# Performance work log

Measured on AMD Instinct MI355X. Metric: run time of the kernel, lower is better.

The kernel has to match this reference:

```python
import jax, jax.numpy as jnp
import numpy as np

EMBED_DIM = 1024
N_HEADS = 16
D_HEAD = EMBED_DIM // N_HEADS


def setup_inputs() -> dict:
    key = jax.random.key(0)
    kx, kq, kk, kv = jax.random.split(key, 4)
    x = jax.random.normal(kx, (2, 2048, EMBED_DIM), dtype=jnp.float32)
    Wq = jax.random.normal(kq, (EMBED_DIM, EMBED_DIM), dtype=jnp.float32) * 0.02
    Wk = jax.random.normal(kk, (EMBED_DIM, EMBED_DIM), dtype=jnp.float32) * 0.02
    Wv = jax.random.normal(kv, (EMBED_DIM, EMBED_DIM), dtype=jnp.float32) * 0.02
    return {"x": x, "Wq": Wq, "Wk": Wk, "Wv": Wv}


def reference(x, Wq, Wk, Wv):
    B, N, D = x.shape
    H, Dh = N_HEADS, D_HEAD
    # Fused QKV projections, then split heads: [B, N, D] -> [B, H, N, Dh]
    q = (x @ Wq).reshape(B, N, H, Dh).transpose(0, 2, 1, 3)
    k = (x @ Wk).reshape(B, N, H, Dh).transpose(0, 2, 1, 3)
    v = (x @ Wv).reshape(B, N, H, Dh).transpose(0, 2, 1, 3)
    scale = 1.0 / jnp.sqrt(jnp.asarray(Dh, dtype=x.dtype))
    scores = jnp.einsum("bhqd,bhkd->bhqk", q, k) * scale  # [B, H, N, N]
    attn = jax.nn.softmax(scores, axis=-1)
    out = jnp.einsum("bhqk,bhkd->bhqd", attn, v)  # [B, H, N, Dh]
    return out.transpose(0, 2, 1, 3).reshape(B, N, D)
```

## Files before the change

kernel.cpp:

```cpp
#include <hip/hip_runtime.h>
#include <cstdint>

typedef __bf16 bf16;
typedef __bf16 bf16x8 __attribute__((ext_vector_type(8)));
typedef float floatx4 __attribute__((ext_vector_type(4)));

typedef const __attribute__((address_space(1))) void* as1_cvptr;
typedef __attribute__((address_space(3))) void* as3_vptr;

__device__ __forceinline__ void gl_lds16(const void* g, void* l) {
  __builtin_amdgcn_global_load_lds((as1_cvptr)(uintptr_t)g,
                                   (as3_vptr)(uint32_t)(uintptr_t)l, 16, 0, 0);
}

#define EMBED 1024
#define SEQ 2048
#define NH 16
#define DH 64

__global__ __launch_bounds__(256) void convert_x(const float* __restrict__ x,
                                                 bf16* __restrict__ xb) {
  int i = (blockIdx.x * 256 + threadIdx.x) * 8;
  floatx4 a = *(const floatx4*)(x + i);
  floatx4 b = *(const floatx4*)(x + i + 4);
  bf16x8 o;
#pragma unroll
  for (int j = 0; j < 4; ++j) { o[j] = (bf16)a[j]; o[4 + j] = (bf16)b[j]; }
  *(bf16x8*)(xb + i) = o;
}

__global__ __launch_bounds__(256) void transpose3(
    const float* __restrict__ Wq, const float* __restrict__ Wk,
    const float* __restrict__ Wv, bf16* __restrict__ Wqt,
    bf16* __restrict__ Wkt, bf16* __restrict__ Wvt) {
  __shared__ __align__(16) bf16 tile[64][72];
  const float* W;
  bf16* Wt;
  if (blockIdx.z == 0) { W = Wq; Wt = Wqt; }
  else if (blockIdx.z == 1) { W = Wk; Wt = Wkt; }
  else { W = Wv; Wt = Wvt; }
  int t = threadIdx.x;
  int k0 = blockIdx.y * 64, n0 = blockIdx.x * 64;
  int r = t >> 3, c = (t & 7) * 8;
#pragma unroll
  for (int half = 0; half < 2; ++half) {
    const float* src = &W[(size_t)(k0 + r + half * 32) * EMBED + n0 + c];
    floatx4 f0 = *(const floatx4*)src;
    floatx4 f1 = *(const floatx4*)(src + 4);
    bf16x8 o;
#pragma unroll
    for (int j = 0; j < 4; ++j) { o[j] = (bf16)f0[j]; o[4 + j] = (bf16)f1[j]; }
    *(bf16x8*)&tile[r + half * 32][c] = o;
  }
  __syncthreads();
#pragma unroll
  for (int p = 0; p < 2; ++p) {
    int nn = (t >> 3) + p * 32, kk = (t & 7) * 8;
    bf16x8 v;
#pragma unroll
    for (int i = 0; i < 8; ++i) v[i] = tile[kk + i][nn];
    *(bf16x8*)&Wt[(size_t)(n0 + nn) * EMBED + k0 + kk] = v;
  }
}

__global__ __launch_bounds__(256) void qkv3(
    const bf16* __restrict__ Xb, const bf16* __restrict__ Wqt,
    const bf16* __restrict__ Wkt, const bf16* __restrict__ Wvt,
    bf16* __restrict__ qo, bf16* __restrict__ ko, bf16* __restrict__ vto) {
  __shared__ __align__(16) bf16 As[128 * 32];
  __shared__ __align__(16) bf16 Bs[128 * 32];

  int gid = blockIdx.x;
  int z = gid % 3;
  int rem = gid / 3;
  int bxx = rem & 7, byy = rem >> 3;

  const bf16* Wt = (z == 0) ? Wqt : (z == 1) ? Wkt : Wvt;
  bf16* out = (z == 0) ? qo : (z == 1) ? ko : vto;
  int m0 = (z == 2 ? bxx : byy) * 128;
  int n0 = (z == 2 ? byy : bxx) * 128;
  const bf16* Asrc = (z == 2) ? Wt : Xb;
  const bf16* Bsrc = (z == 2) ? Xb : Wt;

  int t = threadIdx.x;
  int w = t >> 6, lane = t & 63, ln = lane & 15, quad = lane >> 4;
  int wm = (w >> 1) * 64, wn = (w & 1) * 64;

  floatx4 acc[4][4];
#pragma unroll
  for (int i = 0; i < 4; ++i)
#pragma unroll
    for (int j = 0; j < 4; ++j) acc[i][j] = floatx4{0.f, 0.f, 0.f, 0.f};

  int sr = t >> 2, sc = (t & 3) * 8;
  const bf16* ag = Asrc + (size_t)(m0 + sr) * EMBED + sc;
  const bf16* bg = Bsrc + (size_t)(n0 + sr) * EMBED + sc;
  bf16* al = As + sr * 32 + sc;
  bf16* bl = Bs + sr * 32 + sc;

  for (int k0 = 0; k0 < EMBED; k0 += 32) {
    __syncthreads();
    gl_lds16(ag + k0, al);
    gl_lds16(ag + k0 + (size_t)64 * EMBED, al + 64 * 32);
    gl_lds16(bg + k0, bl);
    gl_lds16(bg + k0 + (size_t)64 * EMBED, bl + 64 * 32);
    __syncthreads();

    bf16x8 afr[4], bfr[4];
#pragma unroll
    for (int i = 0; i < 4; ++i)
      afr[i] = *(const bf16x8*)&As[(wm + i * 16 + ln) * 32 + quad * 8];
#pragma unroll
    for (int j = 0; j < 4; ++j)
      bfr[j] = *(const bf16x8*)&Bs[(wn + j * 16 + ln) * 32 + quad * 8];
#pragma unroll
    for (int i = 0; i < 4; ++i)
#pragma unroll
      for (int j = 0; j < 4; ++j)
        acc[i][j] =
            __builtin_amdgcn_mfma_f32_16x16x32_bf16(afr[i], bfr[j], acc[i][j], 0, 0, 0);
  }

#pragma unroll
  for (int i = 0; i < 4; ++i) {
#pragma unroll
    for (int r = 0; r < 4; ++r) {
      int row = m0 + wm + i * 16 + quad * 4 + r;
#pragma unroll
      for (int j = 0; j < 4; ++j) {
        int col = n0 + wn + j * 16 + ln;
        float v = acc[i][j][r];
        size_t dst;
        if (z != 2) {
          int b = row >> 11, ns = row & 2047, h = col >> 6, d = col & 63;
          dst = ((size_t)((b * NH + h) * SEQ + ns)) * DH + d;
        } else {
          int h = row >> 6, d = row & 63, b = col >> 11, ns = col & 2047;
          dst = ((size_t)((b * NH + h) * DH + d)) * SEQ + ns;
        }
        out[dst] = (bf16)v;
      }
    }
  }
}

__global__ __launch_bounds__(512) void flash(
    const bf16* __restrict__ Qg, const bf16* __restrict__ Kg,
    const bf16* __restrict__ Vtg, float* __restrict__ Og) {
  __shared__ __align__(16) bf16 Ks[128 * 72];
  __shared__ __align__(16) bf16 Vs[64 * 136];
  __shared__ __align__(16) bf16 Ps[8][16 * 136];

  int t = threadIdx.x, w = t >> 6, lane = t & 63, ln = lane & 15, quad = lane >> 4;
  int bh = blockIdx.y;
  int b = bh >> 4, h = bh & 15;
  const bf16* Q = Qg + (size_t)bh * SEQ * DH;
  const bf16* K = Kg + (size_t)bh * SEQ * DH;
  const bf16* Vt = Vtg + (size_t)bh * DH * SEQ;
  int q0 = blockIdx.x * 128 + w * 16;
  const float sl2 = 0.125f * 1.44269504f;

  bf16x8 aq[2];
#pragma unroll
  for (int kc = 0; kc < 2; ++kc)
    aq[kc] = *(const bf16x8*)&Q[(size_t)(q0 + ln) * DH + kc * 32 + quad * 8];

  floatx4 oacc[4];
  float li[4];
#pragma unroll
  for (int dt = 0; dt < 4; ++dt) oacc[dt] = floatx4{0.f, 0.f, 0.f, 0.f};
#pragma unroll
  for (int r = 0; r < 4; ++r) li[r] = 0.f;

  int kr = t >> 3, kcol = (t & 7) * 8;
  int vr = t >> 4, vcol = (t & 15) * 8;
  const bf16* kg = K + (size_t)kr * DH + kcol;
  const bf16* vg = Vt + (size_t)vr * SEQ + vcol;
  bf16* kl = Ks + kr * 72 + kcol;
  bf16* vl = Vs + vr * 136 + vcol;

  bf16x8 pk0 = *(const bf16x8*)(kg);
  bf16x8 pk1 = *(const bf16x8*)(kg + (size_t)64 * DH);
  bf16x8 pv0 = *(const bf16x8*)(vg);
  bf16x8 pv1 = *(const bf16x8*)(vg + (size_t)32 * SEQ);

  for (int kt0 = 0; kt0 < SEQ; kt0 += 128) {
    __syncthreads();
    *(bf16x8*)kl = pk0;
    *(bf16x8*)(kl + 64 * 72) = pk1;
    *(bf16x8*)vl = pv0;
    *(bf16x8*)(vl + 32 * 136) = pv1;
    __syncthreads();

    if (kt0 + 128 < SEQ) {
      int nk = kt0 + 128;
      pk0 = *(const bf16x8*)(kg + (size_t)nk * DH);
      pk1 = *(const bf16x8*)(kg + (size_t)(nk + 64) * DH);
      pv0 = *(const bf16x8*)(vg + nk);
      pv1 = *(const bf16x8*)(vg + (size_t)32 * SEQ + nk);
    }

    floatx4 s[8];
#pragma unroll
    for (int nt = 0; nt < 8; ++nt) s[nt] = floatx4{0.f, 0.f, 0.f, 0.f};
#pragma unroll
    for (int kc = 0; kc < 2; ++kc) {
#pragma unroll
      for (int nt = 0; nt < 8; ++nt) {
        bf16x8 bk = *(const bf16x8*)&Ks[(nt * 16 + ln) * 72 + kc * 32 + quad * 8];
        s[nt] = __builtin_amdgcn_mfma_f32_16x16x32_bf16(aq[kc], bk, s[nt], 0, 0, 0);
      }
    }

#pragma unroll
    for (int r = 0; r < 4; ++r) {
      int prow = quad * 4 + r;
      float lsum = 0.f;
#pragma unroll
      for (int nt = 0; nt < 8; ++nt) {
        float p = exp2f(s[nt][r] * sl2);
        lsum += p;
        Ps[w][prow * 136 + nt * 16 + ln] = (bf16)p;
      }
      li[r] += lsum;
    }

#pragma unroll
    for (int kc2 = 0; kc2 < 4; ++kc2) {
      bf16x8 ap = *(const bf16x8*)&Ps[w][ln * 136 + kc2 * 32 + quad * 8];
#pragma unroll
      for (int dt = 0; dt < 4; ++dt) {
        bf16x8 bv = *(const bf16x8*)&Vs[(dt * 16 + ln) * 136 + kc2 * 32 + quad * 8];
        oacc[dt] = __builtin_amdgcn_mfma_f32_16x16x32_bf16(ap, bv, oacc[dt], 0, 0, 0);
      }
    }
  }

#pragma unroll
  for (int r = 0; r < 4; ++r) {
#pragma unroll
    for (int msk = 1; msk < 16; msk <<= 1) li[r] += __shfl_xor(li[r], msk, 64);
    float inv = 1.0f / li[r];
    int ns = q0 + quad * 4 + r;
#pragma unroll
    for (int dt = 0; dt < 4; ++dt) {
      int d = dt * 16 + ln;
      Og[((size_t)(b * SEQ + ns)) * EMBED + h * DH + d] = oacc[dt][r] * inv;
    }
  }
}

extern "C" void kernel_launch(void* const* d_in, const int* in_sizes, int n_in,
                              void* d_out, int out_size, void* d_ws, size_t ws_size,
                              hipStream_t stream) {
  const int XEL = 2 * 2048 * 1024;
  const float *x, *Wq, *Wk, *Wv;
  if (in_sizes[0] == XEL) {
    x = (const float*)d_in[0];
    Wq = (const float*)d_in[1];
    Wk = (const float*)d_in[2];
    Wv = (const float*)d_in[3];
  } else {
    Wk = (const float*)d_in[0];
    Wq = (const float*)d_in[1];
    Wv = (const float*)d_in[2];
    x = (const float*)d_in[3];
  }
  bf16* ws = (bf16*)d_ws;

  const size_t M1 = 1024 * 1024;
  bf16* q_ws = ws;
  bf16* k_ws = ws + 4 * M1;
  bf16* vt_ws = ws + 8 * M1;
  bf16* wqt = ws + 12 * M1;
  bf16* wkt = ws + 13 * M1;
  bf16* wvt = ws + 14 * M1;
  bf16* xb = ws + 15 * M1;

  convert_x<<<dim3(2048), 256, 0, stream>>>(x, xb);
  transpose3<<<dim3(16, 16, 3), 256, 0, stream>>>(Wq, Wk, Wv, wqt, wkt, wvt);
  qkv3<<<dim3(768), 256, 0, stream>>>(xb, wqt, wkt, wvt, q_ws, k_ws, vt_ws);
  flash<<<dim3(16, 32), 512, 0, stream>>>(q_ws, k_ws, vt_ws, (float*)d_out);
}
```

Before: 183.9 us.

## Merge prep kernels and give each flash wave two query tiles

Fuses the x conversion and the weight transposes into a single prep launch, removing one kernel launch. The flash kernel moves to 256-thread blocks where each wave owns 32 query rows (two 16-row tiles). Each wave reuses its K and V LDS fragments across both tiles and computes S transposed, so P is written as packed bf16x4 stores. The change aims to cut LDS read traffic and per-row reduction overhead, at the cost of more registers per wave and fewer waves per block to hide latency.

Result: no change. 181.1 us (-1.5%).

```diff
diff --git a/kernel.cpp b/kernel.cpp
--- a/kernel.cpp
+++ b/kernel.cpp
@@ -2,6 +2,7 @@
 #include <cstdint>
 
 typedef __bf16 bf16;
+typedef __bf16 bf16x4 __attribute__((ext_vector_type(4)));
 typedef __bf16 bf16x8 __attribute__((ext_vector_type(8)));
 typedef float floatx4 __attribute__((ext_vector_type(4)));
 
@@ -18,29 +19,31 @@
 #define NH 16
 #define DH 64
 
-__global__ __launch_bounds__(256) void convert_x(const float* __restrict__ x,
-                                                 bf16* __restrict__ xb) {
-  int i = (blockIdx.x * 256 + threadIdx.x) * 8;
-  floatx4 a = *(const floatx4*)(x + i);
-  floatx4 b = *(const floatx4*)(x + i + 4);
-  bf16x8 o;
-#pragma unroll
-  for (int j = 0; j < 4; ++j) { o[j] = (bf16)a[j]; o[4 + j] = (bf16)b[j]; }
-  *(bf16x8*)(xb + i) = o;
-}
-
-__global__ __launch_bounds__(256) void transpose3(
-    const float* __restrict__ Wq, const float* __restrict__ Wk,
-    const float* __restrict__ Wv, bf16* __restrict__ Wqt,
+__global__ __launch_bounds__(256) void prep(
+    const float* __restrict__ x, const float* __restrict__ Wq,
+    const float* __restrict__ Wk, const float* __restrict__ Wv,
+    bf16* __restrict__ xb, bf16* __restrict__ Wqt,
     bf16* __restrict__ Wkt, bf16* __restrict__ Wvt) {
   __shared__ __align__(16) bf16 tile[64][72];
-  const float* W;
-  bf16* Wt;
-  if (blockIdx.z == 0) { W = Wq; Wt = Wqt; }
-  else if (blockIdx.z == 1) { W = Wk; Wt = Wkt; }
-  else { W = Wv; Wt = Wvt; }
+  int z = blockIdx.y;
   int t = threadIdx.x;
-  int k0 = blockIdx.y * 64, n0 = blockIdx.x * 64;
+  if (z == 3) {
+    size_t base = ((size_t)blockIdx.x * 256 + t) * 8;
+#pragma unroll
+    for (int it = 0; it < 8; ++it) {
+      size_t i = base + (size_t)it * (256 * 256 * 8);
+      floatx4 a = *(const floatx4*)(x + i);
+      floatx4 bv = *(const floatx4*)(x + i + 4);
+      bf16x8 o;
+#pragma unroll
+      for (int j = 0; j < 4; ++j) { o[j] = (bf16)a[j]; o[4 + j] = (bf16)bv[j]; }
+      *(bf16x8*)(xb + i) = o;
+    }
+    return;
+  }
+  const float* W = (z == 0) ? Wq : (z == 1) ? Wk : Wv;
+  bf16* Wt = (z == 0) ? Wqt : (z == 1) ? Wkt : Wvt;
+  int k0 = (blockIdx.x >> 4) * 64, n0 = (blockIdx.x & 15) * 64;
   int r = t >> 3, c = (t & 7) * 8;
 #pragma unroll
   for (int half = 0; half < 2; ++half) {
@@ -144,12 +147,12 @@
   }
 }
 
-__global__ __launch_bounds__(512) void flash(
+__global__ __launch_bounds__(256) void flash(
     const bf16* __restrict__ Qg, const bf16* __restrict__ Kg,
     const bf16* __restrict__ Vtg, float* __restrict__ Og) {
   __shared__ __align__(16) bf16 Ks[128 * 72];
   __shared__ __align__(16) bf16 Vs[64 * 136];
-  __shared__ __align__(16) bf16 Ps[8][16 * 136];
+  __shared__ __align__(16) bf16 Ps[4][32 * 136];
 
   int t = threadIdx.x, w = t >> 6, lane = t & 63, ln = lane & 15, quad = lane >> 4;
   int bh = blockIdx.y;
@@ -157,20 +160,23 @@
   const bf16* Q = Qg + (size_t)bh * SEQ * DH;
   const bf16* K = Kg + (size_t)bh * SEQ * DH;
   const bf16* Vt = Vtg + (size_t)bh * DH * SEQ;
-  int q0 = blockIdx.x * 128 + w * 16;
+  int q0 = blockIdx.x * 128 + w * 32;
   const float sl2 = 0.125f * 1.44269504f;
 
-  bf16x8 aq[2];
-#pragma unroll
-  for (int kc = 0; kc < 2; ++kc)
-    aq[kc] = *(const bf16x8*)&Q[(size_t)(q0 + ln) * DH + kc * 32 + quad * 8];
-
-  floatx4 oacc[4];
-  float li[4];
-#pragma unroll
-  for (int dt = 0; dt < 4; ++dt) oacc[dt] = floatx4{0.f, 0.f, 0.f, 0.f};
-#pragma unroll
-  for (int r = 0; r < 4; ++r) li[r] = 0.f;
+  bf16x8 bq[2][2];
+#pragma unroll
+  for (int qb = 0; qb < 2; ++qb)
+#pragma unroll
+    for (int kc = 0; kc < 2; ++kc)
+      bq[qb][kc] =
+          *(const bf16x8*)&Q[(size_t)(q0 + qb * 16 + ln) * DH + kc * 32 + quad * 8];
+
+  floatx4 oacc[2][4];
+  float li[2] = {0.f, 0.f};
+#pragma unroll
+  for (int qb = 0; qb < 2; ++qb)
+#pragma unroll
+    for (int dt = 0; dt < 4; ++dt) oacc[qb][dt] = floatx4{0.f, 0.f, 0.f, 0.f};
 
   int kr = t >> 3, kcol = (t & 7) * 8;
   int vr = t >> 4, vcol = (t & 15) * 8;
@@ -179,73 +185,85 @@
   bf16* kl = Ks + kr * 72 + kcol;
   bf16* vl = Vs + vr * 136 + vcol;
 
-  bf16x8 pk0 = *(const bf16x8*)(kg);
-  bf16x8 pk1 = *(const bf16x8*)(kg + (size_t)64 * DH);
-  bf16x8 pv0 = *(const bf16x8*)(vg);
-  bf16x8 pv1 = *(const bf16x8*)(vg + (size_t)32 * SEQ);
+  bf16x8 pk[4], pv[4];
+#pragma unroll
+  for (int p = 0; p < 4; ++p) {
+    pk[p] = *(const bf16x8*)(kg + (size_t)(p * 32) * DH);
+    pv[p] = *(const bf16x8*)(vg + (size_t)(p * 16) * SEQ);
+  }
 
   for (int kt0 = 0; kt0 < SEQ; kt0 += 128) {
     __syncthreads();
-    *(bf16x8*)kl = pk0;
-    *(bf16x8*)(kl + 64 * 72) = pk1;
-    *(bf16x8*)vl = pv0;
-    *(bf16x8*)(vl + 32 * 136) = pv1;
+#pragma unroll
+    for (int p = 0; p < 4; ++p) {
+      *(bf16x8*)(kl + p * 32 * 72) = pk[p];
+      *(bf16x8*)(vl + p * 16 * 136) = pv[p];
+    }
     __syncthreads();
 
     if (kt0 + 128 < SEQ) {
       int nk = kt0 + 128;
-      pk0 = *(const bf16x8*)(kg + (size_t)nk * DH);
-      pk1 = *(const bf16x8*)(kg + (size_t)(nk + 64) * DH);
-      pv0 = *(const bf16x8*)(vg + nk);
-      pv1 = *(const bf16x8*)(vg + (size_t)32 * SEQ + nk);
-    }
-
-    floatx4 s[8];
-#pragma unroll
-    for (int nt = 0; nt < 8; ++nt) s[nt] = floatx4{0.f, 0.f, 0.f, 0.f};
-#pragma unroll
-    for (int kc = 0; kc < 2; ++kc) {
+#pragma unroll
+      for (int p = 0; p < 4; ++p) {
+        pk[p] = *(const bf16x8*)(kg + (size_t)(nk + p * 32) * DH);
+        pv[p] = *(const bf16x8*)(vg + nk + (size_t)(p * 16) * SEQ);
+      }
+    }
+
+#pragma unroll
+    for (int qb = 0; qb < 2; ++qb) {
+      floatx4 s[8];
+#pragma unroll
+      for (int nt = 0; nt < 8; ++nt) s[nt] = floatx4{0.f, 0.f, 0.f, 0.f};
+#pragma unroll
+      for (int kc = 0; kc < 2; ++kc) {
+#pragma unroll
+        for (int nt = 0; nt < 8; ++nt) {
+          bf16x8 ak = *(const bf16x8*)&Ks[(nt * 16 + ln) * 72 + kc * 32 + quad * 8];
+          s[nt] = __builtin_amdgcn_mfma_f32_16x16x32_bf16(ak, bq[qb][kc], s[nt], 0, 0, 0);
+        }
+      }
+      float lacc = 0.f;
 #pragma unroll
       for (int nt = 0; nt < 8; ++nt) {
-        bf16x8 bk = *(const bf16x8*)&Ks[(nt * 16 + ln) * 72 + kc * 32 + quad * 8];
-        s[nt] = __builtin_amdgcn_mfma_f32_16x16x32_bf16(aq[kc], bk, s[nt], 0, 0, 0);
-      }
-    }
-
-#pragma unroll
-    for (int r = 0; r < 4; ++r) {
-      int prow = quad * 4 + r;
-      float lsum = 0.f;
-#pragma unroll
-      for (int nt = 0; nt < 8; ++nt) {
-        float p = exp2f(s[nt][r] * sl2);
-        lsum += p;
-        Ps[w][prow * 136 + nt * 16 + ln] = (bf16)p;
-      }
-      li[r] += lsum;
+        float p0 = exp2f(s[nt][0] * sl2);
+        float p1 = exp2f(s[nt][1] * sl2);
+        float p2 = exp2f(s[nt][2] * sl2);
+        float p3 = exp2f(s[nt][3] * sl2);
+        lacc += (p0 + p1) + (p2 + p3);
+        bf16x4 pq = {(bf16)p0, (bf16)p1, (bf16)p2, (bf16)p3};
+        *(bf16x4*)&Ps[w][(qb * 16 + ln) * 136 + nt * 16 + quad * 4] = pq;
+      }
+      li[qb] += lacc;
     }
 
 #pragma unroll
     for (int kc2 = 0; kc2 < 4; ++kc2) {
-      bf16x8 ap = *(const bf16x8*)&Ps[w][ln * 136 + kc2 * 32 + quad * 8];
+      bf16x8 ap0 = *(const bf16x8*)&Ps[w][ln * 136 + kc2 * 32 + quad * 8];
+      bf16x8 ap1 = *(const bf16x8*)&Ps[w][(16 + ln) * 136 + kc2 * 32 + quad * 8];
 #pragma unroll
       for (int dt = 0; dt < 4; ++dt) {
         bf16x8 bv = *(const bf16x8*)&Vs[(dt * 16 + ln) * 136 + kc2 * 32 + quad * 8];
-        oacc[dt] = __builtin_amdgcn_mfma_f32_16x16x32_bf16(ap, bv, oacc[dt], 0, 0, 0);
-      }
-    }
-  }
-
-#pragma unroll
-  for (int r = 0; r < 4; ++r) {
-#pragma unroll
-    for (int msk = 1; msk < 16; msk <<= 1) li[r] += __shfl_xor(li[r], msk, 64);
-    float inv = 1.0f / li[r];
-    int ns = q0 + quad * 4 + r;
-#pragma unroll
-    for (int dt = 0; dt < 4; ++dt) {
-      int d = dt * 16 + ln;
-      Og[((size_t)(b * SEQ + ns)) * EMBED + h * DH + d] = oacc[dt][r] * inv;
+        oacc[0][dt] = __builtin_amdgcn_mfma_f32_16x16x32_bf16(ap0, bv, oacc[0][dt], 0, 0, 0);
+        oacc[1][dt] = __builtin_amdgcn_mfma_f32_16x16x32_bf16(ap1, bv, oacc[1][dt], 0, 0, 0);
+      }
+    }
+  }
+
+#pragma unroll
+  for (int qb = 0; qb < 2; ++qb) {
+    li[qb] += __shfl_xor(li[qb], 16, 64);
+    li[qb] += __shfl_xor(li[qb], 32, 64);
+    float inv = 1.0f / li[qb];
+#pragma unroll
+    for (int r = 0; r < 4; ++r) {
+      float iv = __shfl(inv, quad * 4 + r, 64);
+      int ns = q0 + qb * 16 + quad * 4 + r;
+#pragma unroll
+      for (int dt = 0; dt < 4; ++dt) {
+        int d = dt * 16 + ln;
+        Og[((size_t)(b * SEQ + ns)) * EMBED + h * DH + d] = oacc[qb][dt][r] * iv;
+      }
     }
   }
 }
@@ -277,8 +295,7 @@
   bf16* wvt = ws + 14 * M1;
   bf16* xb = ws + 15 * M1;
 
-  convert_x<<<dim3(2048), 256, 0, stream>>>(x, xb);
-  transpose3<<<dim3(16, 16, 3), 256, 0, stream>>>(Wq, Wk, Wv, wqt, wkt, wvt);
+  prep<<<dim3(256, 4), 256, 0, stream>>>(x, Wq, Wk, Wv, xb, wqt, wkt, wvt);
   qkv3<<<dim3(768), 256, 0, stream>>>(xb, wqt, wkt, wvt, q_ws, k_ws, vt_ws);
-  flash<<<dim3(16, 32), 512, 0, stream>>>(q_ws, k_ws, vt_ws, (float*)d_out);
-}
+  flash<<<dim3(16, 32), 256, 0, stream>>>(q_ws, k_ws, vt_ws, (float*)d_out);
+}
```
